# Kernel optimization log

Hardware: AMD Instinct MI355X
Metric: run time of the kernel (lower is better)

The kernel has to match this reference:

```python
import jax, jax.numpy as jnp
import numpy as np

B, T, C = 2, 2048, 2048
NH, NKV, HD = 16, 4, 128
GATE_CH = 12
WINDOW = 1024


def apply_rotary_emb(x, cos, sin):
    # x: (B,T,H,HD); cos/sin: (1,T,1,HD//2)
    d = x.shape[3] // 2
    x1, x2 = x[..., :d], x[..., d:]
    return jnp.concatenate([x1 * cos + x2 * sin, -x1 * sin + x2 * cos], axis=3)


def rms_norm(x):
    return x * jax.lax.rsqrt(jnp.mean(jnp.square(x), axis=-1, keepdims=True) + 1e-06)


def setup_inputs() -> dict:
    key = jax.random.key(0)
    ks = jax.random.split(key, 7)
    # realistic RoPE tables
    theta = 10000.0 ** (-jnp.arange(HD // 2, dtype=jnp.float32) / (HD // 2))
    ang = jnp.arange(T, dtype=jnp.float32)[:, None] * theta[None, :]
    cos = jnp.cos(ang)[None, :, None, :]
    sin = jnp.sin(ang)[None, :, None, :]
    return {
        "x": jax.random.normal(ks[0], (B, T, C), jnp.float32),
        "ve": jax.random.normal(ks[1], (B, T, NKV * HD), jnp.float32),
        "cos": cos,
        "sin": sin,
        "Wq": 0.02 * jax.random.normal(ks[2], (NH * HD, C), jnp.float32),
        "Wk": 0.02 * jax.random.normal(ks[3], (NKV * HD, C), jnp.float32),
        "Wv": 0.02 * jax.random.normal(ks[4], (NKV * HD, C), jnp.float32),
        "Wproj": 0.02 * jax.random.normal(ks[5], (C, C), jnp.float32),
        "Wgate": 0.02 * jax.random.normal(ks[6], (NKV, GATE_CH), jnp.float32),
        "window_size": WINDOW,
    }


def reference(x, ve, cos, sin, Wq, Wk, Wv, Wproj, Wgate, window_size):
    B_, T_, C_ = x.shape
    q = (x @ Wq.T).reshape(B_, T_, NH, HD)
    k = (x @ Wk.T).reshape(B_, T_, NKV, HD)
    v = (x @ Wv.T).reshape(B_, T_, NKV, HD)
    # value-embedding gate-add
    gate = 3.0 * jax.nn.sigmoid(x[..., :GATE_CH] @ Wgate.T)  # (B,T,NKV)
    v = v + gate[..., None] * ve.reshape(B_, T_, NKV, HD)
    # RoPE + QK RMSNorm + scale
    q = rms_norm(apply_rotary_emb(q, cos, sin)) * 1.2
    k = rms_norm(apply_rotary_emb(k, cos, sin)) * 1.2
    # GQA head-repeat
    rep = NH // NKV
    k = jnp.repeat(k, rep, axis=2)
    v = jnp.repeat(v, rep, axis=2)
    # sliding-window causal bias (window_size > 0 branch)
    r = jnp.arange(T_)
    mask = (r[None, :] <= r[:, None]) & (r[:, None] - r[None, :] <= window_size)
    bias = jnp.where(mask, 0.0, jnp.finfo(x.dtype).min)  # (T,T)
    scores = jnp.einsum("bthd,bshd->bhts", q, k) * (1.0 / np.sqrt(HD).astype(np.float32))
    scores = scores + bias[None, None, :, :]
    w = jax.nn.softmax(scores, axis=-1)
    y = jnp.einsum("bhts,bshd->bthd", w, v).reshape(B_, T_, -1)
    return y @ Wproj.T
```

## Files before the change

### kernel.cpp

```cpp
#include <hip/hip_runtime.h>
#include <hip/hip_bf16.h>

#define BB   2
#define TT   2048
#define CC   2048
#define NHq  16
#define NKVq 4
#define HDq  128
#define ROWS (BB*TT)
#define NQKV (NHq*HDq + 2*NKVq*HDq)

using bf16 = __hip_bfloat16;
using short8  = __attribute__((ext_vector_type(8))) short;
using short4v = __attribute__((ext_vector_type(4))) short;
using f32x4   = __attribute__((ext_vector_type(4))) float;

#define MFMA16(a,b,c) __builtin_amdgcn_mfma_f32_16x16x32_bf16((a),(b),(c),0,0,0)

__device__ __forceinline__ void gll16(const bf16* g, void* l) {
    __builtin_amdgcn_global_load_lds((const __attribute__((address_space(1))) void*)g,
                                     (__attribute__((address_space(3))) void*)l,
                                     16, 0, 0);
}

__global__ void cast_all(const float* __restrict__ x,  const float* __restrict__ wq,
                         const float* __restrict__ wk, const float* __restrict__ wv,
                         const float* __restrict__ wp, bf16* __restrict__ dst) {
    long e = ((long)blockIdx.x * 256 + threadIdx.x) * 4;
    const float* src; long off;
    if (e < 8388608L)       { src = x;  off = e; }
    else if (e < 12582912L) { src = wq; off = e - 8388608L; }
    else if (e < 13631488L) { src = wk; off = e - 12582912L; }
    else if (e < 14680064L) { src = wv; off = e - 13631488L; }
    else                    { src = wp; off = e - 14680064L; }
    float4 v = *reinterpret_cast<const float4*>(src + off);
    ushort4 o;
    o.x = __bfloat16_as_ushort(__float2bfloat16(v.x));
    o.y = __bfloat16_as_ushort(__float2bfloat16(v.y));
    o.z = __bfloat16_as_ushort(__float2bfloat16(v.z));
    o.w = __bfloat16_as_ushort(__float2bfloat16(v.w));
    *reinterpret_cast<ushort4*>(dst + e) = o;
}

template<int OUT_F32>
__global__ __launch_bounds__(256) void gemm_bt(const bf16* __restrict__ A,
                                               const bf16* __restrict__ B,
                                               void* __restrict__ Cp,
                                               int M, int N, int K) {
    const int bm = blockIdx.x * 128;
    const int bn = blockIdx.y * 128;
    const int tid = threadIdx.x;
    const int lane = tid & 63;
    const int w = tid >> 6;
    const int wr = w >> 1, wc = w & 1;

    __shared__ __align__(16) bf16 As[128 * 64];
    __shared__ __align__(16) bf16 Bs[128 * 64];

    f32x4 acc[4][4];
#pragma unroll
    for (int i = 0; i < 4; ++i)
#pragma unroll
        for (int j = 0; j < 4; ++j) acc[i][j] = f32x4{0.f, 0.f, 0.f, 0.f};

    const int srow = tid >> 3;
    const int sch  = tid & 7;

    const int fr = lane & 15;
    const int kq = lane >> 4;

    for (int k0 = 0; k0 < K; k0 += 64) {
        __syncthreads();
#pragma unroll
        for (int i = 0; i < 4; ++i) {
            int row = i * 32 + srow;
            int c = sch ^ (row & 7);
            gll16(&A[(size_t)(bm + row) * K + k0 + c * 8], (char*)As + i * 4096 + tid * 16);
            gll16(&B[(size_t)(bn + row) * K + k0 + c * 8], (char*)Bs + i * 4096 + tid * 16);
        }
        __syncthreads();

#pragma unroll
        for (int kk = 0; kk < 2; ++kk) {
            short8 af[4], bfr[4];
#pragma unroll
            for (int m = 0; m < 4; ++m) {
                int r = wr * 64 + m * 16 + fr;
                af[m] = *reinterpret_cast<const short8*>(
                    (const char*)As + r * 128 + (((kk * 4 + kq) ^ (r & 7)) * 16));
            }
#pragma unroll
            for (int n = 0; n < 4; ++n) {
                int r = wc * 64 + n * 16 + fr;
                bfr[n] = *reinterpret_cast<const short8*>(
                    (const char*)Bs + r * 128 + (((kk * 4 + kq) ^ (r & 7)) * 16));
            }
            __builtin_amdgcn_s_setprio(1);
#pragma unroll
            for (int m = 0; m < 4; ++m)
#pragma unroll
                for (int n = 0; n < 4; ++n)
                    acc[m][n] = MFMA16(af[m], bfr[n], acc[m][n]);
            __builtin_amdgcn_s_setprio(0);
        }
    }

    const int cr = (lane >> 4) * 4;
    const int cc = lane & 15;
#pragma unroll
    for (int m = 0; m < 4; ++m)
#pragma unroll
        for (int n = 0; n < 4; ++n) {
            int row = bm + wr * 64 + m * 16 + cr;
            int col = bn + wc * 64 + n * 16 + cc;
#pragma unroll
            for (int j = 0; j < 4; ++j) {
                float v = acc[m][n][j];
                if (OUT_F32) ((float*)Cp)[(size_t)(row + j) * N + col] = v;
                else         ((bf16*)Cp)[(size_t)(row + j) * N + col] = __float2bfloat16(v);
            }
        }
}

__global__ __launch_bounds__(256) void postproc(const float* __restrict__ x,
                                                const float* __restrict__ ve,
                                                const float* __restrict__ cosb,
                                                const float* __restrict__ sinb,
                                                const float* __restrict__ Wgate,
                                                bf16* __restrict__ qkv) {
    const int row = blockIdx.x;
    const int t = row & (TT - 1);
    const int tid = threadIdx.x;
    __shared__ float gate_s[NKVq];
    if (tid < NKVq) {
        float g = 0.f;
#pragma unroll
        for (int c = 0; c < 12; ++c) g += x[(size_t)row * CC + c] * Wgate[tid * 12 + c];
        gate_s[tid] = 3.0f / (1.0f + __expf(-g));
    }
    __syncthreads();

    bf16* qkvr = qkv + (size_t)row * NQKV;

#pragma unroll
    for (int i = 0; i < 2; ++i) {
        int idx = tid + i * 256;
        float v = __bfloat162float(qkvr[2560 + idx]);
        v += gate_s[idx >> 7] * ve[(size_t)row * 512 + idx];
        qkvr[2560 + idx] = __float2bfloat16(v);
    }

    const int lane = tid & 63;
    const int w = tid >> 6;
    const float cv = cosb[(size_t)t * 64 + lane];
    const float sv = sinb[(size_t)t * 64 + lane];
    for (int hh = w; hh < NHq + NKVq; hh += 4) {
        int off = (hh < NHq) ? hh * HDq : 2048 + (hh - NHq) * HDq;
        float x1 = __bfloat162float(qkvr[off + lane]);
        float x2 = __bfloat162float(qkvr[off + 64 + lane]);
        float r1 =  x1 * cv + x2 * sv;
        float r2 = -x1 * sv + x2 * cv;
        float ss = r1 * r1 + r2 * r2;
#pragma unroll
        for (int m = 1; m < 64; m <<= 1) ss += __shfl_xor(ss, m);
        float sc = rsqrtf(ss * (1.0f / 128.0f) + 1e-6f) * 1.2f;
        qkvr[off + lane]      = __float2bfloat16(r1 * sc);
        qkvr[off + 64 + lane] = __float2bfloat16(r2 * sc);
    }
}

__global__ __launch_bounds__(256, 2) void attn_mfma(const bf16* __restrict__ qkv,
                                                    bf16* __restrict__ y,
                                                    const int* __restrict__ winp) {
    const int bid = blockIdx.x;
    const int group = bid >> 8, idx = bid & 255;
    const int bh = idx >> 3, jj = idx & 7;
    const int qt = group ? jj : (15 - jj);
    const int h = bh & 15, b = bh >> 4;
    const int t0 = qt * 128;
    const int kvh = h >> 2;
    const int tid = threadIdx.x;
    const int lane = tid & 63;
    const int w = tid >> 6;
    const int window = winp[0];

    __shared__ __align__(16) bf16 Ks[2][64 * 128];
    __shared__ __align__(16) bf16 Vt[128 * 64];
    __shared__ __align__(16) bf16 Ps[4][32 * 64];

    const int fr = lane & 15;
    const int kq = (lane >> 4) * 8;
    const int hi = lane >> 4;

    short8 qf[2][4];
#pragma unroll
    for (int mi = 0; mi < 2; ++mi) {
        const bf16* qp = qkv + ((size_t)(b * TT) + t0 + w * 32 + mi * 16 + fr) * NQKV + h * HDq;
#pragma unroll
        for (int c = 0; c < 4; ++c)
            qf[mi][c] = *reinterpret_cast<const short8*>(&qp[c * 32 + kq]);
    }

    f32x4 acc[2][8];
#pragma unroll
    for (int mi = 0; mi < 2; ++mi)
#pragma unroll
        for (int n = 0; n < 8; ++n) acc[mi][n] = f32x4{0.f, 0.f, 0.f, 0.f};
    float lrow[2][4];
#pragma unroll
    for (int mi = 0; mi < 2; ++mi)
#pragma unroll
        for (int j = 0; j < 4; ++j) lrow[mi][j] = 0.f;

    int s_lo = t0 - window; if (s_lo < 0) s_lo = 0; s_lo &= ~63;
    const int s_end = t0 + 128;

    const bf16* Kg = qkv + (size_t)b * TT * NQKV + 2048 + kvh * HDq;
    const bf16* Vg = Kg + 512;

    const int str = tid >> 4;
    const int sti = tid & 15;
    const int vf  = tid & 15;
    const int vdc = (tid >> 4) * 8;
    const float scl2 = 0.08838834764831845f * 1.4426950408889634f;
    const float CAP = 24.0f;

    short8 vr[4];

#pragma unroll
    for (int p = 0; p < 4; ++p) {
        int row = p * 16 + str;
        int c16 = sti ^ (row & 7);
        gll16(&Kg[(size_t)(s_lo + row) * NQKV + c16 * 8], (char*)Ks + p * 4096 + tid * 16);
    }
#pragma unroll
    for (int i = 0; i < 4; ++i)
        vr[i] = *reinterpret_cast<const short8*>(&Vg[(size_t)(s_lo + 16 * i + vf) * NQKV + vdc]);
#pragma unroll
    for (int j = 0; j < 8; ++j) {
        short4v col;
        col[0] = vr[0][j]; col[1] = vr[1][j]; col[2] = vr[2][j]; col[3] = vr[3][j];
        *reinterpret_cast<short4v*>((char*)Vt + (vdc + j) * 128 + ((8 * vf) ^ (j << 4))) = col;
    }
    __syncthreads();

    int cur = 0;
    for (int sk = s_lo; sk < s_end; sk += 64) {
        const bool hn = (sk + 64 < s_end);
        if (hn) {
#pragma unroll
            for (int p = 0; p < 4; ++p) {
                int row = p * 16 + str;
                int c16 = sti ^ (row & 7);
                gll16(&Kg[(size_t)(sk + 64 + row) * NQKV + c16 * 8],
                      (char*)Ks + (cur ^ 1) * 16384 + p * 4096 + tid * 16);
            }
#pragma unroll
            for (int i = 0; i < 4; ++i)
                vr[i] = *reinterpret_cast<const short8*>(&Vg[(size_t)(sk + 64 + 16 * i + vf) * NQKV + vdc]);
        }

        f32x4 S[2][4];
#pragma unroll
        for (int mi = 0; mi < 2; ++mi)
#pragma unroll
            for (int n = 0; n < 4; ++n) S[mi][n] = f32x4{0.f, 0.f, 0.f, 0.f};
        __builtin_amdgcn_s_setprio(1);
#pragma unroll
        for (int n = 0; n < 4; ++n) {
            int rb = n * 16 + fr;
#pragma unroll
            for (int c = 0; c < 4; ++c) {
                int colb = c * 64 + kq * 2;
                short8 kf = *reinterpret_cast<const short8*>(
                    (const char*)Ks + cur * 16384 + rb * 256 + (colb ^ ((rb & 7) << 4)));
                S[0][n] = MFMA16(qf[0][c], kf, S[0][n]);
                S[1][n] = MFMA16(qf[1][c], kf, S[1][n]);
            }
        }
        __builtin_amdgcn_s_setprio(0);

        const int rw0 = t0 + w * 32;
        const bool interior = (sk + 63 <= rw0) && (rw0 + 31 - sk <= window);
#pragma unroll
        for (int mi = 0; mi < 2; ++mi) {
#pragma unroll
            for (int j = 0; j < 4; ++j) {
                const int rl = hi * 4 + j;
                float s0, s1, s2, s3;
                if (interior) {
                    s0 = S[mi][0][j] * scl2; s1 = S[mi][1][j] * scl2;
                    s2 = S[mi][2][j] * scl2; s3 = S[mi][3][j] * scl2;
                } else {
                    const int r = rw0 + mi * 16 + rl;
                    int c0 = sk + fr, c1 = c0 + 16, c2 = c0 + 32, c3 = c0 + 48;
                    s0 = (c0 <= r && r - c0 <= window) ? S[mi][0][j] * scl2 : -1e30f;
                    s1 = (c1 <= r && r - c1 <= window) ? S[mi][1][j] * scl2 : -1e30f;
                    s2 = (c2 <= r && r - c2 <= window) ? S[mi][2][j] * scl2 : -1e30f;
                    s3 = (c3 <= r && r - c3 <= window) ? S[mi][3][j] * scl2 : -1e30f;
                }
                float p0 = exp2f(s0 - CAP);
                float p1 = exp2f(s1 - CAP);
                float p2 = exp2f(s2 - CAP);
                float p3 = exp2f(s3 - CAP);
                lrow[mi][j] += (p0 + p1) + (p2 + p3);
                short4v pk;
                pk[0] = (short)__bfloat16_as_ushort(__float2bfloat16(p0));
                pk[1] = (short)__bfloat16_as_ushort(__float2bfloat16(p1));
                pk[2] = (short)__bfloat16_as_ushort(__float2bfloat16(p2));
                pk[3] = (short)__bfloat16_as_ushort(__float2bfloat16(p3));
                const int prow = mi * 16 + rl;
                *reinterpret_cast<short4v*>(
                    (char*)Ps + w * 4096 + prow * 128 + ((8 * fr) ^ ((prow & 7) << 4))) = pk;
            }
        }

        __builtin_amdgcn_s_setprio(1);
#pragma unroll
        for (int c2 = 0; c2 < 2; ++c2) {
            short8 pa0 = *reinterpret_cast<const short8*>(
                (char*)Ps + w * 4096 + fr * 128 + ((c2 * 64 + hi * 16) ^ ((fr & 7) << 4)));
            short8 pa1 = *reinterpret_cast<const short8*>(
                (char*)Ps + w * 4096 + (16 + fr) * 128 + ((c2 * 64 + hi * 16) ^ ((fr & 7) << 4)));
#pragma unroll
            for (int n = 0; n < 8; ++n) {
                short8 vb = *reinterpret_cast<const short8*>(
                    (char*)Vt + (n * 16 + fr) * 128 + ((c2 * 64 + hi * 16) ^ ((fr & 7) << 4)));
                acc[0][n] = MFMA16(pa0, vb, acc[0][n]);
                acc[1][n] = MFMA16(pa1, vb, acc[1][n]);
            }
        }
        __builtin_amdgcn_s_setprio(0);

        __syncthreads();
        if (hn) {
#pragma unroll
            for (int j = 0; j < 8; ++j) {
                short4v col;
                col[0] = vr[0][j]; col[1] = vr[1][j]; col[2] = vr[2][j]; col[3] = vr[3][j];
                *reinterpret_cast<short4v*>((char*)Vt + (vdc + j) * 128 + ((8 * vf) ^ (j << 4))) = col;
            }
        }
        __syncthreads();
        cur ^= 1;
    }

#pragma unroll
    for (int mi = 0; mi < 2; ++mi)
#pragma unroll
        for (int j = 0; j < 4; ++j) {
            float l = lrow[mi][j];
#pragma unroll
            for (int mm = 1; mm < 16; mm <<= 1) l += __shfl_xor(l, mm);
            const int r = t0 + w * 32 + mi * 16 + hi * 4 + j;
            float inv = 1.f / l;
            bf16* yr = y + ((size_t)(b * TT) + r) * CC + h * HDq;
#pragma unroll
            for (int n = 0; n < 8; ++n)
                yr[n * 16 + fr] = __float2bfloat16(acc[mi][n][j] * inv);
        }
}

extern "C" void kernel_launch(void* const* d_in, const int* in_sizes, int n_in,
                              void* d_out, int out_size, void* d_ws, size_t ws_size,
                              hipStream_t stream) {
    const float* x     = (const float*)d_in[0];
    const float* ve    = (const float*)d_in[1];
    const float* cosb  = (const float*)d_in[2];
    const float* sinb  = (const float*)d_in[3];
    const float* Wq    = (const float*)d_in[4];
    const float* Wk    = (const float*)d_in[5];
    const float* Wv    = (const float*)d_in[6];
    const float* Wproj = (const float*)d_in[7];
    const float* Wgate = (const float*)d_in[8];
    const int*   winp  = (const int*)d_in[9];

    bf16* xb     = (bf16*)d_ws;
    bf16* wqkvb  = xb + (size_t)ROWS * CC;
    bf16* wprojb = wqkvb + (size_t)NQKV * CC;
    bf16* qkvb   = wprojb + (size_t)CC * CC;
    bf16* yb     = xb;

    cast_all<<<18432, 256, 0, stream>>>(x, Wq, Wk, Wv, Wproj, xb);

    gemm_bt<0><<<dim3(ROWS / 128, NQKV / 128), 256, 0, stream>>>(xb, wqkvb, qkvb, ROWS, NQKV, CC);

    postproc<<<ROWS, 256, 0, stream>>>(x, ve, cosb, sinb, Wgate, qkvb);

    attn_mfma<<<BB * NHq * (TT / 128), 256, 0, stream>>>(qkvb, yb, winp);

    gemm_bt<1><<<dim3(ROWS / 128, CC / 128), 256, 0, stream>>>(yb, wprojb, d_out, ROWS, CC, CC);
}
```

Before: 179.4 us.

## Double-buffer transposed V tile and fold softmax scale into Q

The transposed V tile in LDS is now double-buffered. The next tile's transpose-store moves before the PV MFMAs, which removes one __syncthreads per key block. The softmax scale (1/sqrt(d)·log2e) is applied once to Q fragments in bf16 at load time, so the per-score multiply disappears. This raises LDS use by 16KB per block, which may reduce occupancy at two blocks per SM. Rounding scaled Q to bf16 adds a small precision change.

```diff
diff --git a/kernel.cpp b/kernel.cpp
--- a/kernel.cpp
+++ b/kernel.cpp
@@ -185,20 +185,29 @@
     const int window = winp[0];
 
     __shared__ __align__(16) bf16 Ks[2][64 * 128];
-    __shared__ __align__(16) bf16 Vt[128 * 64];
+    __shared__ __align__(16) bf16 Vt[2][128 * 64];
     __shared__ __align__(16) bf16 Ps[4][32 * 64];
 
     const int fr = lane & 15;
     const int kq = (lane >> 4) * 8;
     const int hi = lane >> 4;
+    const float scl2 = 0.08838834764831845f * 1.4426950408889634f;
+    const float CAP = 24.0f;
 
     short8 qf[2][4];
 #pragma unroll
     for (int mi = 0; mi < 2; ++mi) {
         const bf16* qp = qkv + ((size_t)(b * TT) + t0 + w * 32 + mi * 16 + fr) * NQKV + h * HDq;
 #pragma unroll
-        for (int c = 0; c < 4; ++c)
-            qf[mi][c] = *reinterpret_cast<const short8*>(&qp[c * 32 + kq]);
+        for (int c = 0; c < 4; ++c) {
+            short8 v = *reinterpret_cast<const short8*>(&qp[c * 32 + kq]);
+#pragma unroll
+            for (int e = 0; e < 8; ++e) {
+                float f = __bfloat162float(__ushort_as_bfloat16((ushort)v[e])) * scl2;
+                v[e] = (short)__bfloat16_as_ushort(__float2bfloat16(f));
+            }
+            qf[mi][c] = v;
+        }
     }
 
     f32x4 acc[2][8];
@@ -222,8 +231,6 @@
     const int sti = tid & 15;
     const int vf  = tid & 15;
     const int vdc = (tid >> 4) * 8;
-    const float scl2 = 0.08838834764831845f * 1.4426950408889634f;
-    const float CAP = 24.0f;
 
     short8 vr[4];
 
@@ -231,7 +238,7 @@
     for (int p = 0; p < 4; ++p) {
         int row = p * 16 + str;
         int c16 = sti ^ (row & 7);
-        gll16(&Kg[(size_t)(s_lo + row) * NQKV + c16 * 8], (char*)Ks + p * 4096 + tid * 16);
+        gll16(&Kg[(size_t)(s_lo + row) * NQKV + c16 * 8], (char*)Ks[0] + p * 4096 + tid * 16);
     }
 #pragma unroll
     for (int i = 0; i < 4; ++i)
@@ -240,20 +247,21 @@
     for (int j = 0; j < 8; ++j) {
         short4v col;
         col[0] = vr[0][j]; col[1] = vr[1][j]; col[2] = vr[2][j]; col[3] = vr[3][j];
-        *reinterpret_cast<short4v*>((char*)Vt + (vdc + j) * 128 + ((8 * vf) ^ (j << 4))) = col;
+        *reinterpret_cast<short4v*>((char*)Vt[0] + (vdc + j) * 128 + ((8 * vf) ^ (j << 4))) = col;
     }
     __syncthreads();
 
     int cur = 0;
     for (int sk = s_lo; sk < s_end; sk += 64) {
         const bool hn = (sk + 64 < s_end);
+
         if (hn) {
 #pragma unroll
             for (int p = 0; p < 4; ++p) {
                 int row = p * 16 + str;
                 int c16 = sti ^ (row & 7);
                 gll16(&Kg[(size_t)(sk + 64 + row) * NQKV + c16 * 8],
-                      (char*)Ks + (cur ^ 1) * 16384 + p * 4096 + tid * 16);
+                      (char*)Ks[cur ^ 1] + p * 4096 + tid * 16);
             }
 #pragma unroll
             for (int i = 0; i < 4; ++i)
@@ -273,7 +281,7 @@
             for (int c = 0; c < 4; ++c) {
                 int colb = c * 64 + kq * 2;
                 short8 kf = *reinterpret_cast<const short8*>(
-                    (const char*)Ks + cur * 16384 + rb * 256 + (colb ^ ((rb & 7) << 4)));
+                    (const char*)Ks[cur] + rb * 256 + (colb ^ ((rb & 7) << 4)));
                 S[0][n] = MFMA16(qf[0][c], kf, S[0][n]);
                 S[1][n] = MFMA16(qf[1][c], kf, S[1][n]);
             }
@@ -289,15 +297,15 @@
                 const int rl = hi * 4 + j;
                 float s0, s1, s2, s3;
                 if (interior) {
-                    s0 = S[mi][0][j] * scl2; s1 = S[mi][1][j] * scl2;
-                    s2 = S[mi][2][j] * scl2; s3 = S[mi][3][j] * scl2;
+                    s0 = S[mi][0][j]; s1 = S[mi][1][j];
+                    s2 = S[mi][2][j]; s3 = S[mi][3][j];
                 } else {
                     const int r = rw0 + mi * 16 + rl;
                     int c0 = sk + fr, c1 = c0 + 16, c2 = c0 + 32, c3 = c0 + 48;
-                    s0 = (c0 <= r && r - c0 <= window) ? S[mi][0][j] * scl2 : -1e30f;
-                    s1 = (c1 <= r && r - c1 <= window) ? S[mi][1][j] * scl2 : -1e30f;
-                    s2 = (c2 <= r && r - c2 <= window) ? S[mi][2][j] * scl2 : -1e30f;
-                    s3 = (c3 <= r && r - c3 <= window) ? S[mi][3][j] * scl2 : -1e30f;
+                    s0 = (c0 <= r && r - c0 <= window) ? S[mi][0][j] : -1e30f;
+                    s1 = (c1 <= r && r - c1 <= window) ? S[mi][1][j] : -1e30f;
+                    s2 = (c2 <= r && r - c2 <= window) ? S[mi][2][j] : -1e30f;
+                    s3 = (c3 <= r && r - c3 <= window) ? S[mi][3][j] : -1e30f;
                 }
                 float p0 = exp2f(s0 - CAP);
                 float p1 = exp2f(s1 - CAP);
@@ -315,6 +323,15 @@
             }
         }
 
+        if (hn) {
+#pragma unroll
+            for (int j = 0; j < 8; ++j) {
+                short4v col;
+                col[0] = vr[0][j]; col[1] = vr[1][j]; col[2] = vr[2][j]; col[3] = vr[3][j];
+                *reinterpret_cast<short4v*>((char*)Vt[cur ^ 1] + (vdc + j) * 128 + ((8 * vf) ^ (j << 4))) = col;
+            }
+        }
+
         __builtin_amdgcn_s_setprio(1);
 #pragma unroll
         for (int c2 = 0; c2 < 2; ++c2) {
@@ -325,22 +342,13 @@
 #pragma unroll
             for (int n = 0; n < 8; ++n) {
                 short8 vb = *reinterpret_cast<const short8*>(
-                    (char*)Vt + (n * 16 + fr) * 128 + ((c2 * 64 + hi * 16) ^ ((fr & 7) << 4)));
+                    (char*)Vt[cur] + (n * 16 + fr) * 128 + ((c2 * 64 + hi * 16) ^ ((fr & 7) << 4)));
                 acc[0][n] = MFMA16(pa0, vb, acc[0][n]);
                 acc[1][n] = MFMA16(pa1, vb, acc[1][n]);
             }
         }
         __builtin_amdgcn_s_setprio(0);
 
-        __syncthreads();
-        if (hn) {
-#pragma unroll
-            for (int j = 0; j < 8; ++j) {
-                short4v col;
-                col[0] = vr[0][j]; col[1] = vr[1][j]; col[2] = vr[2][j]; col[3] = vr[3][j];
-                *reinterpret_cast<short4v*>((char*)Vt + (vdc + j) * 128 + ((8 * vf) ^ (j << 4))) = col;
-            }
-        }
         __syncthreads();
         cur ^= 1;
     }
```

Result: no change. 178.4 us (-0.6%).
